# Performance work log

Hardware: AMD Instinct MI355X
Metric: run time of the kernel (lower is better)

Reference implementation:

```python
import jax, jax.numpy as jnp
import numpy as np

NEG_INF = jnp.finfo(jnp.float32).min

def setup_inputs() -> dict:
    key = jax.random.key(0)
    k1, k2, k3, k4 = jax.random.split(key, 4)
    B, H, S, DK, DV = 2, 16, 2048, 64, 64
    Q = jax.random.normal(k1, (B, H, S, DK), dtype=jnp.float32)
    K = jax.random.normal(k2, (B, H, S, DK), dtype=jnp.float32)
    V = jax.random.normal(k3, (B, H, S, DV), dtype=jnp.float32)
    mask = jax.random.randint(k4, (B, 1, S, S), 0, 2, dtype=jnp.int32)
    return {"Q": Q, "K": K, "V": V, "mask": mask}

def reference(Q, K, V, mask):
    d_k = Q.shape[-1]
    # scores: [B, H, Sq, Sk]
    scores = jnp.einsum('bhqd,bhkd->bhqk', Q, K) / jnp.sqrt(jnp.float32(d_k))
    scores = jnp.where(mask == 0, NEG_INF, scores)
    attn_weights = jax.nn.softmax(scores, axis=-1)
    # dropout p=0.0 -> identity (eval-mode reference)
    output = jnp.einsum('bhqk,bhkv->bhqv', attn_weights, V)
    return (output, attn_weights)
```

## Files before the change

### kernel.cpp

```cpp
#include <hip/hip_runtime.h>


typedef __attribute__((ext_vector_type(4))) float f32x4;
typedef __attribute__((ext_vector_type(4))) int   i32x4;

#define S_LEN 2048
#define D_DIM 64
#define H_NUM 16
#define B_NUM 2
#define NT    32
#define SW    32

__device__ __forceinline__ int swz(int row, int colByte) {
  return row * 128 + (colByte ^ ((row & 7) << 4));
}

__device__ __forceinline__ unsigned short f2bf(float f) {
  unsigned int x = __builtin_bit_cast(unsigned int, f);
  x = (x + 0x7FFFu + ((x >> 16) & 1u)) >> 16;
  return (unsigned short)x;
}

__device__ __forceinline__ void mfma16(f32x4& acc, i32x4 a, i32x4 b) {
  asm("v_mfma_f32_16x16x32_bf16 %0, %1, %2, %0" : "+v"(acc) : "v"(a), "v"(b));
}

__global__ __launch_bounds__(256) void mask_pack_kernel(const int* __restrict__ m,
                                                        unsigned long long* __restrict__ bits) {
  const int total = B_NUM * S_LEN * S_LEN;
  const int step  = gridDim.x * blockDim.x;
  for (int i = blockIdx.x * blockDim.x + threadIdx.x; i < total; i += step) {
    unsigned long long b = __ballot(m[i] != 0);
    if ((threadIdx.x & 63) == 0) bits[i >> 6] = b;
  }
}

template <int USE_BITS>
__global__ __launch_bounds__(256) void attn_fwd_kernel(
    const float* __restrict__ Qp, const float* __restrict__ Kp, const float* __restrict__ Vp,
    const unsigned long long* __restrict__ Mb, const int* __restrict__ Mi,
    float* __restrict__ Op, float* __restrict__ Wp)
{
  const int tid  = threadIdx.x;
  const int lane = tid & 63;
  const int wv   = tid >> 6;
  const int l15  = lane & 15;
  const int g4   = lane >> 4;

  const int wg = blockIdx.x;
  const int lg = (wg & 7) * 128 + (wg >> 3);
  const int qt = lg & 31;
  const int bh = lg >> 5;
  const int b  = bh >> 4;

  __shared__ __align__(16) char lds[32768];
  char* Qs  = lds;
  char* Ks  = lds + 8192;
  char* VTs = lds + 16384;
  char* Ps  = lds + 24576 + (wv << 11);

  const float* Qg = Qp + ((size_t)bh * S_LEN + qt * 64) * D_DIM;
  const float* Kg = Kp + (size_t)bh * S_LEN * D_DIM;
  const float* Vg = Vp + (size_t)bh * S_LEN * D_DIM;
  float* Og = Op + ((size_t)bh * S_LEN + qt * 64) * D_DIM;
  float* Wg = Wp + ((size_t)bh * S_LEN + qt * 64) * S_LEN;
  const unsigned long long* Mg = Mb + ((size_t)b * S_LEN + qt * 64) * SW;
  const int* Mig = Mi + ((size_t)b * S_LEN + qt * 64) * S_LEN;

  {
    const int r0 = tid >> 4;
    const int c  = (tid & 15) * 4;
#pragma unroll
    for (int i = 0; i < 4; ++i) {
      const int r = r0 + i * 16;
      float4 v = *(const float4*)(Qg + r * D_DIM + c);
      ushort4 p; p.x = f2bf(v.x); p.y = f2bf(v.y); p.z = f2bf(v.z); p.w = f2bf(v.w);
      *(ushort4*)(Qs + swz(r, c * 2)) = p;
    }
  }
  __syncthreads();
  const i32x4 qa0 = *(const i32x4*)(Qs + swz(wv * 16 + l15, g4 * 16));
  const i32x4 qa1 = *(const i32x4*)(Qs + swz(wv * 16 + l15, g4 * 16 + 64));

  f32x4 oacc[4];
#pragma unroll
  for (int i = 0; i < 4; ++i) oacc[i] = f32x4{0.f, 0.f, 0.f, 0.f};
  float lp[4] = {0.f, 0.f, 0.f, 0.f};

  const int qrow = wv * 16 + g4 * 4;

  for (int kt = 0; kt < NT; ++kt) {
    __syncthreads();
    {
      const int r0 = tid >> 4;
      const int c  = (tid & 15) * 4;
      const float* Kt = Kg + kt * 64 * D_DIM;
#pragma unroll
      for (int i = 0; i < 4; ++i) {
        const int r = r0 + i * 16;
        float4 v = *(const float4*)(Kt + r * D_DIM + c);
        ushort4 p; p.x = f2bf(v.x); p.y = f2bf(v.y); p.z = f2bf(v.z); p.w = f2bf(v.w);
        *(ushort4*)(Ks + swz(r, c * 2)) = p;
      }
      const float* Vt = Vg + kt * 64 * D_DIM;
#pragma unroll
      for (int i = 0; i < 2; ++i) {
        const int rr = (tid >> 4) * 2 + i * 32;
        float4 a  = *(const float4*)(Vt + rr * D_DIM + c);
        float4 bq = *(const float4*)(Vt + (rr + 1) * D_DIM + c);
        const float av[4] = {a.x, a.y, a.z, a.w};
        const float bv[4] = {bq.x, bq.y, bq.z, bq.w};
#pragma unroll
        for (int j = 0; j < 4; ++j) {
          unsigned pk = (unsigned)f2bf(av[j]) | ((unsigned)f2bf(bv[j]) << 16);
          *(unsigned*)(VTs + swz(c + j, rr * 2)) = pk;
        }
      }
    }
    __syncthreads();

    unsigned long long mw[4] = {0, 0, 0, 0};
    if (USE_BITS) {
#pragma unroll
      for (int r = 0; r < 4; ++r) mw[r] = Mg[(qrow + r) * SW + kt];
    }

    f32x4 sacc[4];
#pragma unroll
    for (int i = 0; i < 4; ++i) sacc[i] = f32x4{0.f, 0.f, 0.f, 0.f};
#pragma unroll
    for (int ct = 0; ct < 4; ++ct) {
      i32x4 b0 = *(const i32x4*)(Ks + swz(ct * 16 + l15, g4 * 16));
      i32x4 b1 = *(const i32x4*)(Ks + swz(ct * 16 + l15, g4 * 16 + 64));
      mfma16(sacc[ct], qa0, b0);
      mfma16(sacc[ct], qa1, b1);
    }

#pragma unroll
    for (int ct = 0; ct < 4; ++ct) {
#pragma unroll
      for (int r = 0; r < 4; ++r) {
        float e = __expf(sacc[ct][r] * 0.125f);
        bool keep;
        if (USE_BITS) keep = (mw[r] >> (ct * 16 + l15)) & 1ull;
        else          keep = Mig[(size_t)(qrow + r) * S_LEN + kt * 64 + ct * 16 + l15] != 0;
        e = keep ? e : 0.f;
        lp[r] += e;
        *(unsigned short*)(Ps + swz(g4 * 4 + r, (ct * 16 + l15) * 2)) = f2bf(e);
      }
    }
    asm volatile("s_waitcnt lgkmcnt(0)" ::: "memory");
    __builtin_amdgcn_sched_barrier(0);

    const i32x4 pa0 = *(const i32x4*)(Ps + swz(l15, g4 * 16));
    const i32x4 pa1 = *(const i32x4*)(Ps + swz(l15, g4 * 16 + 64));
#pragma unroll
    for (int ct = 0; ct < 4; ++ct) {
      i32x4 v0 = *(const i32x4*)(VTs + swz(ct * 16 + l15, g4 * 16));
      i32x4 v1 = *(const i32x4*)(VTs + swz(ct * 16 + l15, g4 * 16 + 64));
      mfma16(oacc[ct], pa0, v0);
      mfma16(oacc[ct], pa1, v1);
    }
  }

#pragma unroll
  for (int r = 0; r < 4; ++r) {
    float v = lp[r];
    v += __shfl_xor(v, 1);
    v += __shfl_xor(v, 2);
    v += __shfl_xor(v, 4);
    v += __shfl_xor(v, 8);
    lp[r] = 1.0f / v;
  }

#pragma unroll
  for (int ct = 0; ct < 4; ++ct)
#pragma unroll
    for (int r = 0; r < 4; ++r)
      Og[(size_t)(qrow + r) * D_DIM + ct * 16 + l15] = oacc[ct][r] * lp[r];

  for (int kt = 0; kt < NT; ++kt) {
    __syncthreads();
    {
      const int r0 = tid >> 4;
      const int c  = (tid & 15) * 4;
      const float* Kt = Kg + kt * 64 * D_DIM;
#pragma unroll
      for (int i = 0; i < 4; ++i) {
        const int r = r0 + i * 16;
        float4 v = *(const float4*)(Kt + r * D_DIM + c);
        ushort4 p; p.x = f2bf(v.x); p.y = f2bf(v.y); p.z = f2bf(v.z); p.w = f2bf(v.w);
        *(ushort4*)(Ks + swz(r, c * 2)) = p;
      }
    }
    __syncthreads();

    unsigned long long mw[4] = {0, 0, 0, 0};
    if (USE_BITS) {
#pragma unroll
      for (int r = 0; r < 4; ++r) mw[r] = Mg[(qrow + r) * SW + kt];
    }

    f32x4 sacc[4];
#pragma unroll
    for (int i = 0; i < 4; ++i) sacc[i] = f32x4{0.f, 0.f, 0.f, 0.f};
#pragma unroll
    for (int ct = 0; ct < 4; ++ct) {
      i32x4 b0 = *(const i32x4*)(Ks + swz(ct * 16 + l15, g4 * 16));
      i32x4 b1 = *(const i32x4*)(Ks + swz(ct * 16 + l15, g4 * 16 + 64));
      mfma16(sacc[ct], qa0, b0);
      mfma16(sacc[ct], qa1, b1);
    }

#pragma unroll
    for (int ct = 0; ct < 4; ++ct) {
#pragma unroll
      for (int r = 0; r < 4; ++r) {
        float e = __expf(sacc[ct][r] * 0.125f);
        bool keep;
        if (USE_BITS) keep = (mw[r] >> (ct * 16 + l15)) & 1ull;
        else          keep = Mig[(size_t)(qrow + r) * S_LEN + kt * 64 + ct * 16 + l15] != 0;
        e = keep ? e : 0.f;
        __builtin_nontemporal_store(e * lp[r],
            Wg + (size_t)(qrow + r) * S_LEN + kt * 64 + ct * 16 + l15);
      }
    }
  }
}

extern "C" void kernel_launch(void* const* d_in, const int* in_sizes, int n_in,
                              void* d_out, int out_size, void* d_ws, size_t ws_size,
                              hipStream_t stream) {
  (void)in_sizes; (void)n_in; (void)out_size;
  const float* Q   = (const float*)d_in[0];
  const float* K   = (const float*)d_in[1];
  const float* V   = (const float*)d_in[2];
  const int* mask  = (const int*)d_in[3];
  float* Out = (float*)d_out;
  float* W   = Out + (size_t)B_NUM * H_NUM * S_LEN * D_DIM;

  const size_t bits_bytes = (size_t)(B_NUM * S_LEN * S_LEN / 64) * 8;
  unsigned long long* bits = (unsigned long long*)d_ws;

  if (ws_size >= bits_bytes) {
    mask_pack_kernel<<<1024, 256, 0, stream>>>(mask, bits);
    attn_fwd_kernel<1><<<1024, 256, 0, stream>>>(Q, K, V, bits, mask, Out, W);
  } else {
    attn_fwd_kernel<0><<<1024, 256, 0, stream>>>(Q, K, V, bits, mask, Out, W);
  }
}
```

Measured before the change: 259.5 us.

## Pre-convert Q/K to bf16 and pre-transpose V, load MFMA operands directly from global

Adds pre-pass kernels that convert Q and K to bf16 and write a transposed bf16 copy of V into workspace. A new main kernel then reads MFMA operands straight from global memory (L2) instead of staging K/V tiles through LDS with block barriers, and double-buffers the per-wave P scratch. The goal is to remove the repeated fp32→bf16 conversion of K and V across the 32 query tiles, as well as the per-tile __syncthreads. The cost is extra launches and workspace traffic, plus uncoalesced 16-byte global loads per lane whose latency is no longer hidden by shared staging. It also replaces the inline-asm MFMA with the builtin.

After: 424.8 us. +63.7%, slower.

```diff
diff --git a/kernel.cpp b/kernel.cpp
--- a/kernel.cpp
+++ b/kernel.cpp
@@ -2,7 +2,8 @@
 
 
 typedef __attribute__((ext_vector_type(4))) float f32x4;
-typedef __attribute__((ext_vector_type(4))) int   i32x4;
+typedef __attribute__((ext_vector_type(8))) short s16x8;
+typedef __attribute__((ext_vector_type(4))) unsigned short u16x4;
 
 #define S_LEN 2048
 #define D_DIM 64
@@ -21,9 +22,10 @@
   return (unsigned short)x;
 }
 
-__device__ __forceinline__ void mfma16(f32x4& acc, i32x4 a, i32x4 b) {
-  asm("v_mfma_f32_16x16x32_bf16 %0, %1, %2, %0" : "+v"(acc) : "v"(a), "v"(b));
-}
+__device__ __forceinline__ f32x4 mfma16(f32x4 acc, s16x8 a, s16x8 b) {
+  return __builtin_amdgcn_mfma_f32_16x16x32_bf16(a, b, acc, 0, 0, 0);
+}
+
 
 __global__ __launch_bounds__(256) void mask_pack_kernel(const int* __restrict__ m,
                                                         unsigned long long* __restrict__ bits) {
@@ -34,6 +36,175 @@
     if ((threadIdx.x & 63) == 0) bits[i >> 6] = b;
   }
 }
+
+__global__ __launch_bounds__(256) void cvt_qk_kernel(const float* __restrict__ Q,
+                                                     const float* __restrict__ K,
+                                                     u16x4* __restrict__ Q16,
+                                                     u16x4* __restrict__ K16) {
+  const int n4 = B_NUM * H_NUM * S_LEN * D_DIM / 4;
+  const int step = gridDim.x * blockDim.x;
+  for (int i = blockIdx.x * blockDim.x + threadIdx.x; i < n4; i += step) {
+    float4 q = ((const float4*)Q)[i];
+    Q16[i] = u16x4{f2bf(q.x), f2bf(q.y), f2bf(q.z), f2bf(q.w)};
+    float4 k = ((const float4*)K)[i];
+    K16[i] = u16x4{f2bf(k.x), f2bf(k.y), f2bf(k.z), f2bf(k.w)};
+  }
+}
+
+__global__ __launch_bounds__(256) void v_transpose_kernel(const float* __restrict__ V,
+                                                          unsigned short* __restrict__ VT) {
+  __shared__ unsigned short t[64][72];
+  const int bh = blockIdx.x >> 5;
+  const int st = blockIdx.x & 31;
+  const float* src = V + ((size_t)bh * S_LEN + st * 64) * D_DIM;
+  const int r0 = threadIdx.x >> 4;
+  const int c  = (threadIdx.x & 15) * 4;
+#pragma unroll
+  for (int i = 0; i < 4; ++i) {
+    const int r = r0 + i * 16;
+    float4 v = *(const float4*)(src + r * D_DIM + c);
+    t[c + 0][r] = f2bf(v.x); t[c + 1][r] = f2bf(v.y);
+    t[c + 2][r] = f2bf(v.z); t[c + 3][r] = f2bf(v.w);
+  }
+  __syncthreads();
+#pragma unroll
+  for (int i = 0; i < 4; ++i) {
+    const int idx = threadIdx.x + i * 256;
+    const int d = idx >> 4;
+    const int s4 = (idx & 15) * 4;
+    u16x4 o = {t[d][s4], t[d][s4 + 1], t[d][s4 + 2], t[d][s4 + 3]};
+    *(u16x4*)(VT + ((size_t)bh * D_DIM + d) * S_LEN + st * 64 + s4) = o;
+  }
+}
+
+
+__global__ __launch_bounds__(256) void attn_main_kernel(
+    const unsigned short* __restrict__ Q16, const unsigned short* __restrict__ K16,
+    const unsigned short* __restrict__ VT16, const unsigned long long* __restrict__ Mb,
+    float* __restrict__ Op, float* __restrict__ Wp)
+{
+  const int tid  = threadIdx.x;
+  const int lane = tid & 63;
+  const int wv   = tid >> 6;
+  const int l15  = lane & 15;
+  const int g4   = lane >> 4;
+
+  const int wg = blockIdx.x;
+  const int lg = (wg & 7) * 128 + (wg >> 3);
+  const int qt = lg & 31;
+  const int bh = lg >> 5;
+  const int b  = bh >> 4;
+
+  __shared__ __align__(16) char PsAll[4 * 2 * 2048];
+  char* Ps0 = PsAll + (wv << 12);
+
+  const unsigned short* Qg = Q16 + ((size_t)bh * S_LEN + qt * 64 + wv * 16 + l15) * D_DIM + g4 * 8;
+  const unsigned short* Kg = K16 + (size_t)bh * S_LEN * D_DIM;
+  const unsigned short* Vg = VT16 + (size_t)bh * D_DIM * S_LEN;
+  float* Og = Op + ((size_t)bh * S_LEN + qt * 64) * D_DIM;
+  float* Wg = Wp + ((size_t)bh * S_LEN + qt * 64) * S_LEN;
+  const unsigned long long* Mg = Mb + ((size_t)b * S_LEN + qt * 64) * SW;
+
+  const s16x8 qa0 = *(const s16x8*)Qg;
+  const s16x8 qa1 = *(const s16x8*)(Qg + 32);
+
+  f32x4 oacc[4];
+#pragma unroll
+  for (int i = 0; i < 4; ++i) oacc[i] = f32x4{0.f, 0.f, 0.f, 0.f};
+  float lp[4] = {0.f, 0.f, 0.f, 0.f};
+
+  const int qrow = wv * 16 + g4 * 4;
+
+  for (int kt = 0; kt < NT; ++kt) {
+    char* Ps = Ps0 + ((kt & 1) << 11);
+
+    f32x4 sacc[4];
+#pragma unroll
+    for (int i = 0; i < 4; ++i) sacc[i] = f32x4{0.f, 0.f, 0.f, 0.f};
+#pragma unroll
+    for (int ct = 0; ct < 4; ++ct) {
+      const unsigned short* kp = Kg + (size_t)(kt * 64 + ct * 16 + l15) * D_DIM + g4 * 8;
+      s16x8 b0 = *(const s16x8*)kp;
+      s16x8 b1 = *(const s16x8*)(kp + 32);
+      sacc[ct] = mfma16(sacc[ct], qa0, b0);
+      sacc[ct] = mfma16(sacc[ct], qa1, b1);
+    }
+
+    unsigned long long mw[4];
+#pragma unroll
+    for (int r = 0; r < 4; ++r) mw[r] = Mg[(qrow + r) * SW + kt];
+
+#pragma unroll
+    for (int ct = 0; ct < 4; ++ct) {
+#pragma unroll
+      for (int r = 0; r < 4; ++r) {
+        float e = __expf(sacc[ct][r] * 0.125f);
+        e = ((mw[r] >> (ct * 16 + l15)) & 1ull) ? e : 0.f;
+        lp[r] += e;
+        *(unsigned short*)(Ps + swz(g4 * 4 + r, (ct * 16 + l15) * 2)) = f2bf(e);
+      }
+    }
+    asm volatile("s_waitcnt lgkmcnt(0)" ::: "memory");
+    __builtin_amdgcn_sched_barrier(0);
+
+    const s16x8 pa0 = *(const s16x8*)(Ps + swz(l15, g4 * 16));
+    const s16x8 pa1 = *(const s16x8*)(Ps + swz(l15, g4 * 16 + 64));
+#pragma unroll
+    for (int ct = 0; ct < 4; ++ct) {
+      const unsigned short* vp = Vg + (size_t)(ct * 16 + l15) * S_LEN + kt * 64 + g4 * 8;
+      s16x8 v0 = *(const s16x8*)vp;
+      s16x8 v1 = *(const s16x8*)(vp + 32);
+      oacc[ct] = mfma16(oacc[ct], pa0, v0);
+      oacc[ct] = mfma16(oacc[ct], pa1, v1);
+    }
+  }
+
+#pragma unroll
+  for (int r = 0; r < 4; ++r) {
+    float v = lp[r];
+    v += __shfl_xor(v, 1);
+    v += __shfl_xor(v, 2);
+    v += __shfl_xor(v, 4);
+    v += __shfl_xor(v, 8);
+    lp[r] = 1.0f / v;
+  }
+
+#pragma unroll
+  for (int ct = 0; ct < 4; ++ct)
+#pragma unroll
+    for (int r = 0; r < 4; ++r)
+      Og[(size_t)(qrow + r) * D_DIM + ct * 16 + l15] = oacc[ct][r] * lp[r];
+
+  for (int kt = 0; kt < NT; ++kt) {
+    f32x4 sacc[4];
+#pragma unroll
+    for (int i = 0; i < 4; ++i) sacc[i] = f32x4{0.f, 0.f, 0.f, 0.f};
+#pragma unroll
+    for (int ct = 0; ct < 4; ++ct) {
+      const unsigned short* kp = Kg + (size_t)(kt * 64 + ct * 16 + l15) * D_DIM + g4 * 8;
+      s16x8 b0 = *(const s16x8*)kp;
+      s16x8 b1 = *(const s16x8*)(kp + 32);
+      sacc[ct] = mfma16(sacc[ct], qa0, b0);
+      sacc[ct] = mfma16(sacc[ct], qa1, b1);
+    }
+
+    unsigned long long mw[4];
+#pragma unroll
+    for (int r = 0; r < 4; ++r) mw[r] = Mg[(qrow + r) * SW + kt];
+
+#pragma unroll
+    for (int ct = 0; ct < 4; ++ct) {
+#pragma unroll
+      for (int r = 0; r < 4; ++r) {
+        float e = __expf(sacc[ct][r] * 0.125f);
+        e = ((mw[r] >> (ct * 16 + l15)) & 1ull) ? e : 0.f;
+        __builtin_nontemporal_store(e * lp[r],
+            Wg + (size_t)(qrow + r) * S_LEN + kt * 64 + ct * 16 + l15);
+      }
+    }
+  }
+}
+
 
 template <int USE_BITS>
 __global__ __launch_bounds__(256) void attn_fwd_kernel(
@@ -79,8 +250,8 @@
     }
   }
   __syncthreads();
-  const i32x4 qa0 = *(const i32x4*)(Qs + swz(wv * 16 + l15, g4 * 16));
-  const i32x4 qa1 = *(const i32x4*)(Qs + swz(wv * 16 + l15, g4 * 16 + 64));
+  const s16x8 qa0 = *(const s16x8*)(Qs + swz(wv * 16 + l15, g4 * 16));
+  const s16x8 qa1 = *(const s16x8*)(Qs + swz(wv * 16 + l15, g4 * 16 + 64));
 
   f32x4 oacc[4];
 #pragma unroll
@@ -130,10 +301,10 @@
     for (int i = 0; i < 4; ++i) sacc[i] = f32x4{0.f, 0.f, 0.f, 0.f};
 #pragma unroll
     for (int ct = 0; ct < 4; ++ct) {
-      i32x4 b0 = *(const i32x4*)(Ks + swz(ct * 16 + l15, g4 * 16));
-      i32x4 b1 = *(const i32x4*)(Ks + swz(ct * 16 + l15, g4 * 16 + 64));
-      mfma16(sacc[ct], qa0, b0);
-      mfma16(sacc[ct], qa1, b1);
+      s16x8 b0 = *(const s16x8*)(Ks + swz(ct * 16 + l15, g4 * 16));
+      s16x8 b1 = *(const s16x8*)(Ks + swz(ct * 16 + l15, g4 * 16 + 64));
+      sacc[ct] = mfma16(sacc[ct], qa0, b0);
+      sacc[ct] = mfma16(sacc[ct], qa1, b1);
     }
 
 #pragma unroll
@@ -152,14 +323,14 @@
     asm volatile("s_waitcnt lgkmcnt(0)" ::: "memory");
     __builtin_amdgcn_sched_barrier(0);
 
-    const i32x4 pa0 = *(const i32x4*)(Ps + swz(l15, g4 * 16));
-    const i32x4 pa1 = *(const i32x4*)(Ps + swz(l15, g4 * 16 + 64));
-#pragma unroll
-    for (int ct = 0; ct < 4; ++ct) {
-      i32x4 v0 = *(const i32x4*)(VTs + swz(ct * 16 + l15, g4 * 16));
-      i32x4 v1 = *(const i32x4*)(VTs + swz(ct * 16 + l15, g4 * 16 + 64));
-      mfma16(oacc[ct], pa0, v0);
-      mfma16(oacc[ct], pa1, v1);
+    const s16x8 pa0 = *(const s16x8*)(Ps + swz(l15, g4 * 16));
+    const s16x8 pa1 = *(const s16x8*)(Ps + swz(l15, g4 * 16 + 64));
+#pragma unroll
+    for (int ct = 0; ct < 4; ++ct) {
+      s16x8 v0 = *(const s16x8*)(VTs + swz(ct * 16 + l15, g4 * 16));
+      s16x8 v1 = *(const s16x8*)(VTs + swz(ct * 16 + l15, g4 * 16 + 64));
+      oacc[ct] = mfma16(oacc[ct], pa0, v0);
+      oacc[ct] = mfma16(oacc[ct], pa1, v1);
     }
   }
 
@@ -206,10 +377,10 @@
     for (int i = 0; i < 4; ++i) sacc[i] = f32x4{0.f, 0.f, 0.f, 0.f};
 #pragma unroll
     for (int ct = 0; ct < 4; ++ct) {
-      i32x4 b0 = *(const i32x4*)(Ks + swz(ct * 16 + l15, g4 * 16));
-      i32x4 b1 = *(const i32x4*)(Ks + swz(ct * 16 + l15, g4 * 16 + 64));
-      mfma16(sacc[ct], qa0, b0);
-      mfma16(sacc[ct], qa1, b1);
+      s16x8 b0 = *(const s16x8*)(Ks + swz(ct * 16 + l15, g4 * 16));
+      s16x8 b1 = *(const s16x8*)(Ks + swz(ct * 16 + l15, g4 * 16 + 64));
+      sacc[ct] = mfma16(sacc[ct], qa0, b0);
+      sacc[ct] = mfma16(sacc[ct], qa1, b1);
     }
 
 #pragma unroll
@@ -240,9 +411,18 @@
   float* W   = Out + (size_t)B_NUM * H_NUM * S_LEN * D_DIM;
 
   const size_t bits_bytes = (size_t)(B_NUM * S_LEN * S_LEN / 64) * 8;
+  const size_t t16_bytes  = (size_t)B_NUM * H_NUM * S_LEN * D_DIM * 2;
   unsigned long long* bits = (unsigned long long*)d_ws;
 
-  if (ws_size >= bits_bytes) {
+  if (ws_size >= bits_bytes + 3 * t16_bytes) {
+    unsigned short* Q16 = (unsigned short*)((char*)d_ws + bits_bytes);
+    unsigned short* K16 = Q16 + t16_bytes / 2;
+    unsigned short* VT  = K16 + t16_bytes / 2;
+    mask_pack_kernel<<<1024, 256, 0, stream>>>(mask, bits);
+    cvt_qk_kernel<<<2048, 256, 0, stream>>>(Q, K, (u16x4*)Q16, (u16x4*)K16);
+    v_transpose_kernel<<<1024, 256, 0, stream>>>(V, VT);
+    attn_main_kernel<<<1024, 256, 0, stream>>>(Q16, K16, VT, bits, Out, W);
+  } else if (ws_size >= bits_bytes) {
     mask_pack_kernel<<<1024, 256, 0, stream>>>(mask, bits);
     attn_fwd_kernel<1><<<1024, 256, 0, stream>>>(Q, K, V, bits, mask, Out, W);
   } else {
```
